# Kernel optimization log

Measured on AMD Instinct MI355X. Metric: run time of the kernel, lower is better.

## Reference

```python
import jax, jax.numpy as jnp
import numpy as np

B, T, S, H = 4, 2048, 2048, 1024


def setup_inputs() -> dict:
    key = jax.random.key(0)
    k1, k2, k3, k4, k5, k6 = jax.random.split(key, 6)
    scale_w = 1.0 / np.sqrt(H)  # roughly nn.Linear init scale
    return {
        "tar": jax.random.normal(k1, (B, T, H), jnp.float32),
        "src": jax.random.normal(k2, (B, S, H), jnp.float32),
        "ori_src": jax.random.normal(k3, (B, S, H), jnp.float32),
        "Wq": jax.random.normal(k4, (H, H), jnp.float32) * scale_w,
        "Wk": jax.random.normal(k5, (H, H), jnp.float32) * scale_w,
        "Wv": jax.random.normal(k6, (H, H), jnp.float32) * scale_w,
    }


def reference(tar, src, ori_src, Wq, Wk, Wv):
    # nn.Linear(bias=False): y = x @ W.T
    q = src @ Wq.T        # (B, S, H)
    k = tar @ Wk.T        # (B, T, H)
    v = ori_src @ Wv.T    # (B, S, H)
    scaling = jnp.asarray(H ** 0.5, q.dtype)
    # scores[b,t,s] = q[b,s] . k[b,t] / sqrt(H); torch softmax was over dim=-2 (the S axis)
    scores = jnp.einsum('bsh,bth->bts', q, k) / scaling  # (B, T, S)
    attn = jax.nn.softmax(scores, axis=-1)               # softmax over src positions s
    context = jnp.einsum('bts,bsh->bth', attn, v)        # (B, T, H)
    return context, attn
```

## Files before the change

### kernel.cpp

```cpp
#include <hip/hip_runtime.h>

#define BB 4
#define TT 2048
#define SS 2048
#define HH 1024

typedef unsigned short u16;
typedef __attribute__((ext_vector_type(4))) unsigned short u16x4;
typedef __attribute__((ext_vector_type(8))) short bf16x8;
typedef __attribute__((ext_vector_type(4))) float f32x4;

#define TILE_U16 (128 * 32)

__device__ __forceinline__ u16 f2bf(float f) {
    union { float f; unsigned u; } a; a.f = f;
    unsigned r = a.u + 0x7fffu + ((a.u >> 16) & 1u);
    return (u16)(r >> 16);
}
__device__ __forceinline__ float bf2f(u16 h) {
    union { unsigned u; float f; } a; a.u = ((unsigned)h) << 16;
    return a.f;
}

__device__ __forceinline__ void stage_bf16(const u16* gbase, int ld, int row0, int k0,
                                           u16* lds, int tid) {
#pragma unroll
    for (int c = 0; c < 2; ++c) {
        int g = c * 256 + tid;
        int row = g >> 2, col = g & 3;
        const u16* gp = gbase + (size_t)(row0 + row) * ld + k0 + col * 8;
        u16* lp = lds + (size_t)(c * 256 + (tid & ~63)) * 8;
        __builtin_amdgcn_global_load_lds((__attribute__((address_space(1))) const void*)gp,
                                         (__attribute__((address_space(3))) void*)lp,
                                         16, 0, 0);
    }
}

__device__ __forceinline__ void stage_f32(const float* gbase, int ld, int row0, int k0,
                                          u16* lds, int tid) {
#pragma unroll
    for (int c = 0; c < 4; ++c) {
        int f = c * 256 + tid;
        int row = f >> 3, c4 = f & 7;
        const float4 v = *(const float4*)(gbase + (size_t)(row0 + row) * ld + k0 + c4 * 4);
        u16x4 o;
        o.x = f2bf(v.x); o.y = f2bf(v.y); o.z = f2bf(v.z); o.w = f2bf(v.w);
        *(u16x4*)(lds + row * 32 + c4 * 4) = o;
    }
}

__device__ __forceinline__ void mfma_step(const u16* As, const u16* Bs,
                                          f32x4 acc[4][4], int tid) {
    int lane = tid & 63, quad = lane >> 4, l16 = lane & 15;
    int wm = (tid >> 6) & 1, wn = tid >> 7;
    const u16* Ab = As + (wm * 64 + l16) * 32 + quad * 8;
    const u16* Bb = Bs + (wn * 64 + l16) * 32 + quad * 8;
    bf16x8 af[4], bfr[4];
#pragma unroll
    for (int i = 0; i < 4; ++i) af[i] = *(const bf16x8*)(Ab + i * 512);
#pragma unroll
    for (int j = 0; j < 4; ++j) bfr[j] = *(const bf16x8*)(Bb + j * 512);
#pragma unroll
    for (int i = 0; i < 4; ++i)
#pragma unroll
        for (int j = 0; j < 4; ++j)
            acc[i][j] = __builtin_amdgcn_mfma_f32_16x16x32_bf16(af[i], bfr[j], acc[i][j], 0, 0, 0);
}

__device__ __forceinline__ void zero_acc(f32x4 acc[4][4]) {
#pragma unroll
    for (int i = 0; i < 4; ++i)
#pragma unroll
        for (int j = 0; j < 4; ++j)
            acc[i][j] = (f32x4){0.f, 0.f, 0.f, 0.f};
}

__device__ __forceinline__ void gemm_loop_bf16(const u16* A, int lda, int bm,
                                               const u16* B, int ldb, int bn,
                                               int K, u16* As, u16* Bs,
                                               f32x4 acc[4][4], int tid) {
    stage_bf16(A, lda, bm, 0, As, tid);
    stage_bf16(B, ldb, bn, 0, Bs, tid);
    const int kiters = K / 32;
    for (int kit = 0; kit < kiters; ++kit) {
        const int cur = (kit & 1) * TILE_U16, nxt = TILE_U16 - cur;
        __syncthreads();
        if (kit + 1 < kiters) {
            stage_bf16(A, lda, bm, (kit + 1) * 32, As + nxt, tid);
            stage_bf16(B, ldb, bn, (kit + 1) * 32, Bs + nxt, tid);
        }
        mfma_step(As + cur, Bs + cur, acc, tid);
    }
}

__device__ __forceinline__ void gemm_loop_f32a(const float* A, int lda, int bm,
                                               const u16* B, int ldb, int bn,
                                               int K, u16* As, u16* Bs,
                                               f32x4 acc[4][4], int tid) {
    stage_f32(A, lda, bm, 0, As, tid);
    stage_bf16(B, ldb, bn, 0, Bs, tid);
    const int kiters = K / 32;
    for (int kit = 0; kit < kiters; ++kit) {
        const int cur = (kit & 1) * TILE_U16, nxt = TILE_U16 - cur;
        __syncthreads();
        if (kit + 1 < kiters) {
            stage_f32(A, lda, bm, (kit + 1) * 32, As + nxt, tid);
            stage_bf16(B, ldb, bn, (kit + 1) * 32, Bs + nxt, tid);
        }
        mfma_step(As + cur, Bs + cur, acc, tid);
    }
}

__global__ __launch_bounds__(256) void cvt3_kernel(const float* __restrict__ p0,
                                                   const float* __restrict__ p1,
                                                   const float* __restrict__ p2,
                                                   u16* __restrict__ o0,
                                                   u16* __restrict__ o1,
                                                   u16* __restrict__ o2) {
    const int z = blockIdx.y;
    const float* in = (z == 0) ? p0 : (z == 1) ? p1 : p2;
    u16* out = (z == 0) ? o0 : (z == 1) ? o1 : o2;
    int i = (blockIdx.x * 256 + threadIdx.x) * 4;
    float4 v = *(const float4*)(in + i);
    u16x4 o;
    o.x = f2bf(v.x); o.y = f2bf(v.y); o.z = f2bf(v.z); o.w = f2bf(v.w);
    *(u16x4*)(out + i) = o;
}

__global__ __launch_bounds__(256) void cvt_kernel(const float* __restrict__ in,
                                                  u16* __restrict__ out) {
    int i = (blockIdx.x * 256 + threadIdx.x) * 4;
    float4 v = *(const float4*)(in + i);
    u16x4 o;
    o.x = f2bf(v.x); o.y = f2bf(v.y); o.z = f2bf(v.z); o.w = f2bf(v.w);
    *(u16x4*)(out + i) = o;
}

__global__ __launch_bounds__(256) void zero_kernel(float* __restrict__ p) {
    int i = (blockIdx.x * 256 + threadIdx.x) * 4;
    *(float4*)(p + i) = (float4){0.f, 0.f, 0.f, 0.f};
}

template <int AF32, int NZ>
__global__ __launch_bounds__(256, 4) void proj_kernel(const float* __restrict__ F0,
                                                      const float* __restrict__ F1,
                                                      const float* __restrict__ F2,
                                                      const u16* __restrict__ A0,
                                                      const u16* __restrict__ A1,
                                                      const u16* __restrict__ A2,
                                                      const u16* __restrict__ W0,
                                                      const u16* __restrict__ W1,
                                                      const u16* __restrict__ W2,
                                                      u16* __restrict__ qb,
                                                      u16* __restrict__ kb,
                                                      u16* __restrict__ vT,
                                                      int zbase) {
    __shared__ u16 As[2 * TILE_U16];
    __shared__ u16 Bs[2 * TILE_U16];
    const int bid = blockIdx.x;
    const int xcd = bid & 7, slot = bid >> 3;
    const int bx = slot & 7;
    const int grp = xcd * (NZ * 8) + (slot >> 3);
    const int z = zbase + (NZ == 3 ? (grp >> 6) : 0);
    const int by = grp & 63;

    const float* AF = (z == 0) ? F0 : (z == 1) ? F1 : F2;
    const u16* AB = (z == 0) ? A0 : (z == 1) ? A1 : A2;
    const u16* W = (z == 0) ? W0 : (z == 1) ? W1 : W2;
    const int bm = by * 128, bn = bx * 128;
    const int tid = threadIdx.x;

    f32x4 acc[4][4];
    zero_acc(acc);
    if (AF32) gemm_loop_f32a(AF, HH, bm, W, HH, bn, HH, As, Bs, acc, tid);
    else      gemm_loop_bf16(AB, HH, bm, W, HH, bn, HH, As, Bs, acc, tid);

    const int lane = tid & 63, quad = lane >> 4, l16 = lane & 15;
    const int wm = (tid >> 6) & 1, wn = tid >> 7;
    const int m0 = bm + wm * 64, n0 = bn + wn * 64;
    if (z < 2) {
        u16* C = (z == 0) ? qb : kb;
#pragma unroll
        for (int i = 0; i < 4; ++i)
#pragma unroll
            for (int j = 0; j < 4; ++j) {
                int m = m0 + i * 16 + quad * 4;
                int n = n0 + j * 16 + l16;
#pragma unroll
                for (int r = 0; r < 4; ++r)
                    C[(size_t)(m + r) * HH + n] = f2bf(acc[i][j][r]);
            }
    } else {
#pragma unroll
        for (int i = 0; i < 4; ++i)
#pragma unroll
            for (int j = 0; j < 4; ++j) {
                int m = m0 + i * 16 + quad * 4;
                int n = n0 + j * 16 + l16;
                u16x4 o;
                o.x = f2bf(acc[i][j][0]); o.y = f2bf(acc[i][j][1]);
                o.z = f2bf(acc[i][j][2]); o.w = f2bf(acc[i][j][3]);
                *(u16x4*)(vT + (size_t)n * (BB * SS) + m) = o;
            }
    }
}

template <int FUSE>
__global__ __launch_bounds__(256, 4) void scores_kernel(const u16* __restrict__ qb,
                                                        const u16* __restrict__ kb,
                                                        float* __restrict__ attn,
                                                        u16* __restrict__ eb,
                                                        float* __restrict__ rowsum) {
    __shared__ u16 As[2 * TILE_U16];
    __shared__ u16 Bs[2 * TILE_U16];
    const int bid = blockIdx.x;
    const int xcd = bid & 7, slot = bid >> 3;
    const int bx = slot & 15;
    const int grp = xcd * 8 + (slot >> 4);
    const int b = grp >> 4, by = grp & 15;

    const u16* A = kb + (size_t)b * TT * HH;
    const u16* Bq = qb + (size_t)b * SS * HH;
    const int bm = by * 128, bn = bx * 128;
    const int tid = threadIdx.x;

    f32x4 acc[4][4];
    zero_acc(acc);
    gemm_loop_bf16(A, HH, bm, Bq, HH, bn, HH, As, Bs, acc, tid);

    const int lane = tid & 63, quad = lane >> 4, l16 = lane & 15;
    const int wm = (tid >> 6) & 1, wn = tid >> 7;
    const int m0 = bm + wm * 64, n0 = bn + wn * 64;

    if (FUSE) {
#pragma unroll
        for (int i = 0; i < 4; ++i)
#pragma unroll
            for (int j = 0; j < 4; ++j)
#pragma unroll
                for (int r = 0; r < 4; ++r)
                    acc[i][j][r] = __expf(acc[i][j][r] * 0.03125f);
        u16* E = eb + (size_t)b * TT * SS;
#pragma unroll
        for (int i = 0; i < 4; ++i)
#pragma unroll
            for (int j = 0; j < 4; ++j) {
                int m = m0 + i * 16 + quad * 4;
                int n = n0 + j * 16 + l16;
#pragma unroll
                for (int r = 0; r < 4; ++r)
                    E[(size_t)(m + r) * SS + n] = f2bf(acc[i][j][r]);
            }
        const size_t Rb = (size_t)b * TT + m0 + quad * 4;
#pragma unroll
        for (int i = 0; i < 4; ++i)
#pragma unroll
            for (int r = 0; r < 4; ++r) {
                float s = acc[i][0][r] + acc[i][1][r] + acc[i][2][r] + acc[i][3][r];
                s += __shfl_xor(s, 1, 64);
                s += __shfl_xor(s, 2, 64);
                s += __shfl_xor(s, 4, 64);
                s += __shfl_xor(s, 8, 64);
                if (l16 == 0) atomicAdd(&rowsum[Rb + i * 16 + r], s);
            }
    } else {
        float* C = attn + (size_t)b * TT * SS;
#pragma unroll
        for (int i = 0; i < 4; ++i)
#pragma unroll
            for (int j = 0; j < 4; ++j) {
                int m = m0 + i * 16 + quad * 4;
                int n = n0 + j * 16 + l16;
#pragma unroll
                for (int r = 0; r < 4; ++r)
                    C[(size_t)(m + r) * SS + n] = acc[i][j][r] * 0.03125f;
            }
    }
}

__global__ __launch_bounds__(256) void norm_kernel(const u16* __restrict__ eb,
                                                   const float* __restrict__ rowsum,
                                                   float* __restrict__ attn) {
    const size_t row = blockIdx.x;
    const float inv = 1.0f / rowsum[row];
    const u16* p = eb + row * SS;
    float* o = attn + row * SS;
    const int tid = threadIdx.x;
#pragma unroll
    for (int c = 0; c < 2; ++c) {
        u16x4 v = *(const u16x4*)(p + c * 1024 + tid * 4);
        float4 f;
        f.x = bf2f(v.x) * inv; f.y = bf2f(v.y) * inv;
        f.z = bf2f(v.z) * inv; f.w = bf2f(v.w) * inv;
        *(float4*)(o + c * 1024 + tid * 4) = f;
    }
}

__global__ __launch_bounds__(256) void softmax_kernel(float* __restrict__ attn,
                                                      u16* __restrict__ attn_bf) {
    const size_t row = blockIdx.x;
    float* p = attn + row * SS;
    const int tid = threadIdx.x;
    float4 a = *(float4*)(p + tid * 4);
    float4 b = *(float4*)(p + 1024 + tid * 4);

    float m = fmaxf(fmaxf(fmaxf(a.x, a.y), fmaxf(a.z, a.w)),
                    fmaxf(fmaxf(b.x, b.y), fmaxf(b.z, b.w)));
#pragma unroll
    for (int off = 32; off > 0; off >>= 1) m = fmaxf(m, __shfl_xor(m, off, 64));
    __shared__ float rmax[4], rsum[4];
    if ((tid & 63) == 0) rmax[tid >> 6] = m;
    __syncthreads();
    m = fmaxf(fmaxf(rmax[0], rmax[1]), fmaxf(rmax[2], rmax[3]));

    a.x = __expf(a.x - m); a.y = __expf(a.y - m);
    a.z = __expf(a.z - m); a.w = __expf(a.w - m);
    b.x = __expf(b.x - m); b.y = __expf(b.y - m);
    b.z = __expf(b.z - m); b.w = __expf(b.w - m);
    float s = a.x + a.y + a.z + a.w + b.x + b.y + b.z + b.w;
#pragma unroll
    for (int off = 32; off > 0; off >>= 1) s += __shfl_xor(s, off, 64);
    if ((tid & 63) == 0) rsum[tid >> 6] = s;
    __syncthreads();
    s = rsum[0] + rsum[1] + rsum[2] + rsum[3];
    float inv = 1.0f / s;

    a.x *= inv; a.y *= inv; a.z *= inv; a.w *= inv;
    b.x *= inv; b.y *= inv; b.z *= inv; b.w *= inv;
    *(float4*)(p + tid * 4) = a;
    *(float4*)(p + 1024 + tid * 4) = b;

    if (attn_bf) {
        u16* pb = attn_bf + row * SS;
        u16x4 oa, ob;
        oa.x = f2bf(a.x); oa.y = f2bf(a.y); oa.z = f2bf(a.z); oa.w = f2bf(a.w);
        ob.x = f2bf(b.x); ob.y = f2bf(b.y); ob.z = f2bf(b.z); ob.w = f2bf(b.w);
        *(u16x4*)(pb + tid * 4) = oa;
        *(u16x4*)(pb + 1024 + tid * 4) = ob;
    }
}

template <int AF32, int SCALE>
__global__ __launch_bounds__(256, 4) void ctx_kernel(const float* __restrict__ attnF,
                                                     const u16* __restrict__ attnB,
                                                     const u16* __restrict__ vT,
                                                     const float* __restrict__ rowsum,
                                                     float* __restrict__ out) {
    __shared__ u16 As[2 * TILE_U16];
    __shared__ u16 Bs[2 * TILE_U16];
    const int bid = blockIdx.x;
    const int xcd = bid & 7, slot = bid >> 3;
    const int bx = slot & 7;
    const int grp = xcd * 8 + (slot >> 3);
    const int b = grp >> 4, by = grp & 15;

    const float* AF = attnF + (size_t)b * TT * SS;
    const u16* AB = attnB + (size_t)b * TT * SS;
    const u16* Bv = vT + (size_t)b * SS;
    float* C = out + (size_t)b * TT * HH;
    const int bm = by * 128, bn = bx * 128;
    const int tid = threadIdx.x;

    f32x4 acc[4][4];
    zero_acc(acc);
    if (AF32) gemm_loop_f32a(AF, SS, bm, Bv, BB * SS, bn, SS, As, Bs, acc, tid);
    else      gemm_loop_bf16(AB, SS, bm, Bv, BB * SS, bn, SS, As, Bs, acc, tid);

    const int lane = tid & 63, quad = lane >> 4, l16 = lane & 15;
    const int wm = (tid >> 6) & 1, wn = tid >> 7;
    const int m0 = bm + wm * 64, n0 = bn + wn * 64;
#pragma unroll
    for (int i = 0; i < 4; ++i)
#pragma unroll
        for (int r = 0; r < 4; ++r) {
            int m = m0 + i * 16 + quad * 4 + r;
            float scl = 1.0f;
            if (SCALE) scl = 1.0f / rowsum[(size_t)b * TT + m];
#pragma unroll
            for (int j = 0; j < 4; ++j) {
                int n = n0 + j * 16 + l16;
                C[(size_t)m * HH + n] = acc[i][j][r] * scl;
            }
        }
}

extern "C" void kernel_launch(void* const* d_in, const int* in_sizes, int n_in,
                              void* d_out, int out_size, void* d_ws, size_t ws_size,
                              hipStream_t stream) {
    const float* tar = (const float*)d_in[0];
    const float* src = (const float*)d_in[1];
    const float* ori = (const float*)d_in[2];
    const float* Wq  = (const float*)d_in[3];
    const float* Wk  = (const float*)d_in[4];
    const float* Wv  = (const float*)d_in[5];

    float* ctx_out  = (float*)d_out;
    float* attn_out = ctx_out + (size_t)BB * TT * HH;

    const size_t M1 = 1024 * 1024;
    u16* ws  = (u16*)d_ws;
    u16* qb  = ws;
    u16* kb  = ws + 8 * M1;
    u16* vT  = ws + 16 * M1;
    u16* wqb = ws + 24 * M1;
    u16* wkb = ws + 25 * M1;
    u16* wvb = ws + 26 * M1;
    u16* inb = ws + 27 * M1;
    u16* eb = inb;
    float* rowsum = (float*)wqb;
    u16* attn_bf = qb;

    const size_t need_fused = (27 + 24) * M1 * 2;
    const size_t need_split = (27 + 8) * M1 * 2;
    const int mode = (ws_size >= need_fused) ? 0 : (ws_size >= need_split) ? 1 : 2;

    cvt3_kernel<<<dim3(1024, 3), 256, 0, stream>>>(Wq, Wk, Wv, wqb, wkb, wvb);

    if (mode == 0) {
        u16* srcb = inb;
        u16* tarb = inb + 8 * M1;
        u16* orib = inb + 16 * M1;
        cvt3_kernel<<<dim3(8192, 3), 256, 0, stream>>>(src, tar, ori, srcb, tarb, orib);
        proj_kernel<0, 3><<<1536, 256, 0, stream>>>(
            nullptr, nullptr, nullptr, srcb, tarb, orib, wqb, wkb, wvb, qb, kb, vT, 0);
    } else if (mode == 1) {
        const float* fin[3] = {src, tar, ori};
        for (int z = 0; z < 3; ++z) {
            cvt_kernel<<<8192, 256, 0, stream>>>(fin[z], inb);
            proj_kernel<0, 1><<<512, 256, 0, stream>>>(
                nullptr, nullptr, nullptr, inb, inb, inb, wqb, wkb, wvb, qb, kb, vT, z);
        }
    } else {
        proj_kernel<1, 3><<<1536, 256, 0, stream>>>(
            src, tar, ori, nullptr, nullptr, nullptr, wqb, wkb, wvb, qb, kb, vT, 0);
    }

    if (mode == 0) {
        zero_kernel<<<8, 256, 0, stream>>>(rowsum);
        scores_kernel<1><<<1024, 256, 0, stream>>>(qb, kb, nullptr, eb, rowsum);
        norm_kernel<<<BB * TT, 256, 0, stream>>>(eb, rowsum, attn_out);
        ctx_kernel<0, 1><<<512, 256, 0, stream>>>(nullptr, eb, vT, rowsum, ctx_out);
    } else {
        scores_kernel<0><<<1024, 256, 0, stream>>>(qb, kb, attn_out, nullptr, nullptr);
        softmax_kernel<<<BB * TT, 256, 0, stream>>>(attn_out,
                                                    (mode < 2) ? attn_bf : nullptr);
        if (mode < 2) {
            ctx_kernel<0, 0><<<512, 256, 0, stream>>>(nullptr, attn_bf, vT, nullptr, ctx_out);
        } else {
            ctx_kernel<1, 0><<<512, 256, 0, stream>>>(attn_out, nullptr, vT, nullptr, ctx_out);
        }
    }
}
```

Before: 358.8 us.

## Add 256-row tiled GEMM core with swizzled LDS and use it for projection, scores, ctx

Adds a new GEMM main loop with 512 threads per block and 256xBN tiles, using K=64 stages. LDS is XOR-swizzled to avoid bank conflicts. Barriers are interleaved with prefetch, MFMA runs at raised priority, and workgroup order is remapped so each XCD shares data. The fused-workspace path now uses it for the projection, score/exp and context GEMMs instead of the older 128-tile kernels, to raise data reuse and MFMA utilisation. It depends on hand-placed waitcnt counts, and the larger tiles mean fewer blocks and higher register pressure.

```diff
diff --git a/kernel.cpp b/kernel.cpp
--- a/kernel.cpp
+++ b/kernel.cpp
@@ -21,6 +21,7 @@
     union { unsigned u; float f; } a; a.u = ((unsigned)h) << 16;
     return a.f;
 }
+
 
 __device__ __forceinline__ void stage_bf16(const u16* gbase, int ld, int row0, int k0,
                                            u16* lds, int tid) {
@@ -110,6 +111,7 @@
         mfma_step(As + cur, Bs + cur, acc, tid);
     }
 }
+
 
 __global__ __launch_bounds__(256) void cvt3_kernel(const float* __restrict__ p0,
                                                    const float* __restrict__ p1,
@@ -140,6 +142,241 @@
     int i = (blockIdx.x * 256 + threadIdx.x) * 4;
     *(float4*)(p + i) = (float4){0.f, 0.f, 0.f, 0.f};
 }
+
+
+__device__ __forceinline__ void stage_half(const u16* g, int ld, u16* lds, int tid) {
+#pragma unroll
+    for (int c = 0; c < 2; ++c) {
+        int gr = c * 512 + tid;
+        int r = gr >> 3, k8 = gr & 7;
+        const u16* gp = g + (size_t)r * ld + ((k8 ^ (r & 7)) << 3);
+        u16* lp = lds + (size_t)(c * 512 + (tid & ~63)) * 8;
+        __builtin_amdgcn_global_load_lds((__attribute__((address_space(1))) const void*)gp,
+                                         (__attribute__((address_space(3))) void*)lp,
+                                         16, 0, 0);
+    }
+}
+
+#define G256_RD_A(qm)                                                         \
+    _Pragma("unroll") for (int i = 0; i < 4; ++i) {                           \
+        const u16* _p = Ab + ((qm) * 64 + i * 16 + l16) * 64;                 \
+        a[i][0] = *(const bf16x8*)(_p + co0);                                 \
+        a[i][1] = *(const bf16x8*)(_p + co1);                                 \
+    }
+
+#define G256_RD_B(qn)                                                         \
+    _Pragma("unroll") for (int j = 0; j < J2; ++j) {                          \
+        const u16* _p = Bb + (rB0 + (qn) * J2 * 16 + j * 16 + l16) * 64;      \
+        b[j][0] = *(const bf16x8*)(_p + co0);                                 \
+        b[j][1] = *(const bf16x8*)(_p + co1);                                 \
+    }
+
+#define G256_MFMA(qm, qn)                                                     \
+    __builtin_amdgcn_s_barrier();                                             \
+    asm volatile("s_waitcnt lgkmcnt(0)" ::: "memory");                        \
+    __builtin_amdgcn_s_setprio(1);                                            \
+    _Pragma("unroll") for (int i = 0; i < 4; ++i)                             \
+        _Pragma("unroll") for (int j = 0; j < J2; ++j) {                      \
+            acc[(qm) * 4 + i][(qn) * J2 + j] =                                \
+                __builtin_amdgcn_mfma_f32_16x16x32_bf16(                      \
+                    a[i][0], b[j][0], acc[(qm) * 4 + i][(qn) * J2 + j], 0, 0, 0); \
+            acc[(qm) * 4 + i][(qn) * J2 + j] =                                \
+                __builtin_amdgcn_mfma_f32_16x16x32_bf16(                      \
+                    a[i][1], b[j][1], acc[(qm) * 4 + i][(qn) * J2 + j], 0, 0, 0); \
+        }                                                                     \
+    __builtin_amdgcn_s_setprio(0);
+
+template <int BN>
+__device__ __forceinline__ void g256_loop(const u16* __restrict__ A, int lda,
+                                          const u16* __restrict__ B, int ldb, int K,
+                                          u16* sm, f32x4 (&acc)[8][BN / 64], int tid) {
+    constexpr int J2 = BN / 128;
+    constexpr int ATILE = 16384;
+    constexpr int BTILE = BN * 64;
+    u16* As = sm;
+    u16* Bs = sm + 2 * ATILE;
+    const int lane = tid & 63, wid = tid >> 6;
+    const int wm = wid >> 2, wn = wid & 3;
+    const int l16 = lane & 15, quad = lane >> 4;
+    const int co0 = (quad ^ (l16 & 7)) * 8;
+    const int co1 = ((4 | quad) ^ (l16 & 7)) * 8;
+    const int rB0 = (BN == 256) ? (wn & 1) * 64 : wn * 32;
+    const int NT = K >> 6;
+
+#pragma unroll
+    for (int i = 0; i < 8; ++i)
+#pragma unroll
+        for (int j = 0; j < BN / 64; ++j) acc[i][j] = (f32x4){0.f, 0.f, 0.f, 0.f};
+
+    stage_half(A, lda, As, tid);
+    stage_half(A + (size_t)128 * lda, lda, As + 8192, tid);
+    stage_half(B, ldb, Bs, tid);
+    if (BN == 256) stage_half(B + (size_t)128 * ldb, ldb, Bs + 8192, tid);
+    stage_half(A + 64, lda, As + ATILE, tid);
+    stage_half(A + (size_t)128 * lda + 64, lda, As + ATILE + 8192, tid);
+    asm volatile("s_waitcnt vmcnt(4)" ::: "memory");
+    __builtin_amdgcn_s_barrier();
+    __builtin_amdgcn_sched_barrier(0);
+
+    const u16* Aw = As + wm * 8192;
+    const u16* Bw = Bs + ((BN == 256) ? (wn >> 1) * 8192 : 0);
+
+    for (int t = 0; t < NT; ++t) {
+        const u16* Ab = Aw + (t & 1) * ATILE;
+        const u16* Bb = Bw + (t & 1) * BTILE;
+        const int nx = (t + 1) & 1;
+        bf16x8 a[4][2], b[J2][2];
+        G256_RD_A(0)
+        G256_RD_B(0)
+        if (t + 1 < NT) stage_half(B + (size_t)(t + 1) * 64, ldb, Bs + nx * BTILE, tid);
+        G256_MFMA(0, 0)
+        __builtin_amdgcn_s_barrier();
+        G256_RD_B(1)
+        if (BN == 256 && t + 1 < NT)
+            stage_half(B + (size_t)128 * ldb + (size_t)(t + 1) * 64, ldb,
+                       Bs + nx * BTILE + 8192, tid);
+        G256_MFMA(0, 1)
+        __builtin_amdgcn_s_barrier();
+        G256_RD_A(1)
+        G256_MFMA(1, 1)
+        __builtin_amdgcn_s_barrier();
+        G256_RD_B(0)
+        if (t + 2 < NT) {
+            stage_half(A + (size_t)(t + 2) * 64, lda, As + (t & 1) * ATILE, tid);
+            stage_half(A + (size_t)128 * lda + (size_t)(t + 2) * 64, lda,
+                       As + (t & 1) * ATILE + 8192, tid);
+        }
+        G256_MFMA(1, 0)
+        if (t + 2 < NT) asm volatile("s_waitcnt vmcnt(4)" ::: "memory");
+        else            asm volatile("s_waitcnt vmcnt(0)" ::: "memory");
+        __builtin_amdgcn_s_barrier();
+        __builtin_amdgcn_sched_barrier(0);
+    }
+}
+
+__global__ __launch_bounds__(512, 2) void proj256_kernel(
+        const u16* __restrict__ A0, const u16* __restrict__ A1, const u16* __restrict__ A2,
+        const u16* __restrict__ W0, const u16* __restrict__ W1, const u16* __restrict__ W2,
+        u16* __restrict__ qb, u16* __restrict__ kb, u16* __restrict__ vT) {
+    __shared__ u16 sm[2 * 16384 + 2 * 128 * 64];
+    const int bid = blockIdx.x;
+    const int wg = (bid & 7) * 96 + (bid >> 3);
+    const int z = wg >> 8, rr = wg & 255;
+    const int by = rr >> 3, bx = rr & 7;
+    const u16* A = ((z == 0) ? A0 : (z == 1) ? A1 : A2) + (size_t)(by * 256) * HH;
+    const u16* W = ((z == 0) ? W0 : (z == 1) ? W1 : W2) + (size_t)(bx * 128) * HH;
+    const int tid = threadIdx.x;
+    f32x4 acc[8][2];
+    g256_loop<128>(A, HH, W, HH, HH, sm, acc, tid);
+
+    const int lane = tid & 63, quad = lane >> 4, l16 = lane & 15, wid = tid >> 6;
+    const int wm = wid >> 2, wn = wid & 3;
+    const int m0 = by * 256 + wm * 128, n0 = bx * 128 + wn * 32;
+    if (z < 2) {
+        u16* C = z ? kb : qb;
+#pragma unroll
+        for (int i = 0; i < 8; ++i)
+#pragma unroll
+            for (int j = 0; j < 2; ++j) {
+                const int m = m0 + i * 16 + quad * 4;
+                const int n = n0 + j * 16 + l16;
+#pragma unroll
+                for (int r = 0; r < 4; ++r)
+                    C[(size_t)(m + r) * HH + n] = f2bf(acc[i][j][r]);
+            }
+    } else {
+#pragma unroll
+        for (int i = 0; i < 8; ++i)
+#pragma unroll
+            for (int j = 0; j < 2; ++j) {
+                const int m = m0 + i * 16 + quad * 4;
+                const int n = n0 + j * 16 + l16;
+                u16x4 o;
+                o.x = f2bf(acc[i][j][0]); o.y = f2bf(acc[i][j][1]);
+                o.z = f2bf(acc[i][j][2]); o.w = f2bf(acc[i][j][3]);
+                *(u16x4*)(vT + (size_t)n * (BB * SS) + m) = o;
+            }
+    }
+}
+
+__global__ __launch_bounds__(512, 2) void scores256_kernel(
+        const u16* __restrict__ qb, const u16* __restrict__ kb,
+        u16* __restrict__ eb, float* __restrict__ rowsum) {
+    __shared__ u16 sm[2 * 16384 + 2 * 256 * 64];
+    const int bid = blockIdx.x;
+    const int wg = (bid & 7) * 32 + (bid >> 3);
+    const int b = wg >> 6, by = (wg >> 3) & 7, bx = wg & 7;
+    const u16* A = kb + (size_t)b * TT * HH + (size_t)(by * 256) * HH;
+    const u16* Q = qb + (size_t)b * SS * HH + (size_t)(bx * 256) * HH;
+    const int tid = threadIdx.x;
+    f32x4 acc[8][4];
+    g256_loop<256>(A, HH, Q, HH, HH, sm, acc, tid);
+
+    const int lane = tid & 63, quad = lane >> 4, l16 = lane & 15, wid = tid >> 6;
+    const int wm = wid >> 2, wn = wid & 3;
+    const int m0 = by * 256 + wm * 128, n0 = bx * 256 + wn * 64;
+#pragma unroll
+    for (int i = 0; i < 8; ++i)
+#pragma unroll
+        for (int j = 0; j < 4; ++j)
+#pragma unroll
+            for (int r = 0; r < 4; ++r)
+                acc[i][j][r] = __expf(acc[i][j][r] * 0.03125f);
+    u16* E = eb + (size_t)b * TT * SS;
+#pragma unroll
+    for (int i = 0; i < 8; ++i)
+#pragma unroll
+        for (int j = 0; j < 4; ++j) {
+            const int m = m0 + i * 16 + quad * 4;
+            const int n = n0 + j * 16 + l16;
+#pragma unroll
+            for (int r = 0; r < 4; ++r)
+                E[(size_t)(m + r) * SS + n] = f2bf(acc[i][j][r]);
+        }
+    const size_t Rb = (size_t)b * TT + m0 + quad * 4;
+#pragma unroll
+    for (int i = 0; i < 8; ++i)
+#pragma unroll
+        for (int r = 0; r < 4; ++r) {
+            float s = acc[i][0][r] + acc[i][1][r] + acc[i][2][r] + acc[i][3][r];
+            s += __shfl_xor(s, 1, 64);
+            s += __shfl_xor(s, 2, 64);
+            s += __shfl_xor(s, 4, 64);
+            s += __shfl_xor(s, 8, 64);
+            if (l16 == 0) atomicAdd(&rowsum[Rb + i * 16 + r], s);
+        }
+}
+
+__global__ __launch_bounds__(512, 2) void ctx256_kernel(
+        const u16* __restrict__ eb, const u16* __restrict__ vT,
+        const float* __restrict__ rowsum, float* __restrict__ out) {
+    __shared__ u16 sm[2 * 16384 + 2 * 128 * 64];
+    const int bid = blockIdx.x;
+    const int wg = (bid & 7) * 32 + (bid >> 3);
+    const int b = wg >> 6, by = (wg >> 3) & 7, bx = wg & 7;
+    const u16* A = eb + (size_t)b * TT * SS + (size_t)(by * 256) * SS;
+    const u16* V = vT + (size_t)b * SS + (size_t)(bx * 128) * (size_t)(BB * SS);
+    const int tid = threadIdx.x;
+    f32x4 acc[8][2];
+    g256_loop<128>(A, SS, V, BB * SS, SS, sm, acc, tid);
+
+    const int lane = tid & 63, quad = lane >> 4, l16 = lane & 15, wid = tid >> 6;
+    const int wm = wid >> 2, wn = wid & 3;
+    const int m0 = by * 256 + wm * 128, n0 = bx * 128 + wn * 32;
+    float* C = out + (size_t)b * TT * HH;
+    const float* RS = rowsum + (size_t)b * TT;
+#pragma unroll
+    for (int i = 0; i < 8; ++i)
+#pragma unroll
+        for (int r = 0; r < 4; ++r) {
+            const int m = m0 + i * 16 + quad * 4 + r;
+            const float scl = 1.0f / RS[m];
+#pragma unroll
+            for (int j = 0; j < 2; ++j)
+                C[(size_t)m * HH + n0 + j * 16 + l16] = acc[i][j][r] * scl;
+        }
+}
+
 
 template <int AF32, int NZ>
 __global__ __launch_bounds__(256, 4) void proj_kernel(const float* __restrict__ F0,
@@ -421,8 +658,11 @@
         u16* tarb = inb + 8 * M1;
         u16* orib = inb + 16 * M1;
         cvt3_kernel<<<dim3(8192, 3), 256, 0, stream>>>(src, tar, ori, srcb, tarb, orib);
-        proj_kernel<0, 3><<<1536, 256, 0, stream>>>(
-            nullptr, nullptr, nullptr, srcb, tarb, orib, wqb, wkb, wvb, qb, kb, vT, 0);
+        proj256_kernel<<<768, 512, 0, stream>>>(srcb, tarb, orib, wqb, wkb, wvb, qb, kb, vT);
+        zero_kernel<<<8, 256, 0, stream>>>(rowsum);
+        scores256_kernel<<<256, 512, 0, stream>>>(qb, kb, eb, rowsum);
+        norm_kernel<<<BB * TT, 256, 0, stream>>>(eb, rowsum, attn_out);
+        ctx256_kernel<<<256, 512, 0, stream>>>(eb, vT, rowsum, ctx_out);
     } else if (mode == 1) {
         const float* fin[3] = {src, tar, ori};
         for (int z = 0; z < 3; ++z) {
@@ -430,24 +670,14 @@
             proj_kernel<0, 1><<<512, 256, 0, stream>>>(
                 nullptr, nullptr, nullptr, inb, inb, inb, wqb, wkb, wvb, qb, kb, vT, z);
         }
+        scores_kernel<0><<<1024, 256, 0, stream>>>(qb, kb, attn_out, nullptr, nullptr);
+        softmax_kernel<<<BB * TT, 256, 0, stream>>>(attn_out, attn_bf);
+        ctx_kernel<0, 0><<<512, 256, 0, stream>>>(nullptr, attn_bf, vT, nullptr, ctx_out);
     } else {
         proj_kernel<1, 3><<<1536, 256, 0, stream>>>(
             src, tar, ori, nullptr, nullptr, nullptr, wqb, wkb, wvb, qb, kb, vT, 0);
-    }
-
-    if (mode == 0) {
-        zero_kernel<<<8, 256, 0, stream>>>(rowsum);
-        scores_kernel<1><<<1024, 256, 0, stream>>>(qb, kb, nullptr, eb, rowsum);
-        norm_kernel<<<BB * TT, 256, 0, stream>>>(eb, rowsum, attn_out);
-        ctx_kernel<0, 1><<<512, 256, 0, stream>>>(nullptr, eb, vT, rowsum, ctx_out);
-    } else {
         scores_kernel<0><<<1024, 256, 0, stream>>>(qb, kb, attn_out, nullptr, nullptr);
-        softmax_kernel<<<BB * TT, 256, 0, stream>>>(attn_out,
-                                                    (mode < 2) ? attn_bf : nullptr);
-        if (mode < 2) {
-            ctx_kernel<0, 0><<<512, 256, 0, stream>>>(nullptr, attn_bf, vT, nullptr, ctx_out);
-        } else {
-            ctx_kernel<1, 0><<<512, 256, 0, stream>>>(attn_out, nullptr, vT, nullptr, ctx_out);
-        }
-    }
-}
+        softmax_kernel<<<BB * TT, 256, 0, stream>>>(attn_out, nullptr);
+        ctx_kernel<1, 0><<<512, 256, 0, stream>>>(attn_out, nullptr, vT, nullptr, ctx_out);
+    }
+}
```

Measured after the change: 348.5 us. 2.8% less time.
